# Optimization experiments

Hardware: AMD Instinct MI355X
Metric: run time of the kernel (lower is better)

Reference implementation:

```python
import jax, jax.numpy as jnp
import numpy as np


def _lstm(x_seq, Wih, Whh, bih, bhh, hidden):
    """Single-layer batch_first LSTM, PyTorch gate order (i,f,g,o).
    x_seq: [B, T, D_in]. Returns (outputs [B, T, H], h_T [B, H])."""
    B = x_seq.shape[0]
    h0 = jnp.zeros((B, hidden), x_seq.dtype)
    c0 = jnp.zeros((B, hidden), x_seq.dtype)

    def step(carry, x_t):
        h, c = carry
        gates = x_t @ Wih.T + bih + h @ Whh.T + bhh  # [B, 4H]
        i, f, g, o = jnp.split(gates, 4, axis=-1)
        i = jax.nn.sigmoid(i)
        f = jax.nn.sigmoid(f)
        g = jnp.tanh(g)
        o = jax.nn.sigmoid(o)
        c = f * c + i * g
        h = o * jnp.tanh(c)
        return (h, c), h

    (hT, _), hs = jax.lax.scan(step, (h0, c0), jnp.swapaxes(x_seq, 0, 1))
    return jnp.swapaxes(hs, 0, 1), hT


def setup_inputs() -> dict:
    key = jax.random.key(0)
    ks = jax.random.split(key, 20)
    B, T = 4096, 140
    W = 0.1  # weight scale to keep gates out of saturation
    inp = {"x": jax.random.normal(ks[0], (B, 1, T), jnp.float32)}
    shapes = {
        "Wih_e1": (512, 1), "Whh_e1": (512, 128), "bih_e1": (512,), "bhh_e1": (512,),
        "Wih_e2": (256, 128), "Whh_e2": (256, 64), "bih_e2": (256,), "bhh_e2": (256,),
        "Wih_d1": (512, 64), "Whh_d1": (512, 128), "bih_d1": (512,), "bhh_d1": (512,),
        "Wih_d2": (4, 128), "Whh_d2": (4, 1), "bih_d2": (4,), "bhh_d2": (4,),
    }
    for i, (name, shp) in enumerate(shapes.items()):
        inp[name] = jax.random.normal(ks[i + 1], shp, jnp.float32) * W
    return inp


def reference(x, Wih_e1, Whh_e1, bih_e1, bhh_e1,
              Wih_e2, Whh_e2, bih_e2, bhh_e2,
              Wih_d1, Whh_d1, bih_d1, bhh_d1,
              Wih_d2, Whh_d2, bih_d2, bhh_d2):
    T = 140
    # x: [B,1,140] -> [B,140,1]
    x_enc = x[:, 0, :, None]
    _, h1 = _lstm(x_enc, Wih_e1, Whh_e1, bih_e1, bhh_e1, 128)  # h1: [B,128]
    # faithful to original bug: hn1 [1,B,128] fed as batch_first input (batch=1, seq=B)
    hn1_seq = h1[None, :, :]
    _, z = _lstm(hn1_seq, Wih_e2, Whh_e2, bih_e2, bhh_e2, 64)  # z: [1,64]
    dec_in = jnp.broadcast_to(z[:, None, :], (1, T, 64))
    out1, _ = _lstm(dec_in, Wih_d1, Whh_d1, bih_d1, bhh_d1, 128)  # [1,140,128]
    out2, _ = _lstm(out1, Wih_d2, Whh_d2, bih_d2, bhh_d2, 1)      # [1,140,1]
    recon = out2[..., 0][:, None, :]  # [1,1,140]
    return recon
```

## Files before the change

kernel.cpp:

```cpp
#include <hip/hip_runtime.h>
#include <hip/hip_bf16.h>


typedef float v2f __attribute__((ext_vector_type(2)));

__device__ __forceinline__ v2f pk_fma(v2f a, v2f b, v2f c) {
  v2f d;
  asm("v_pk_fma_f32 %0, %1, %2, %3" : "=v"(d) : "v"(a), "v"(b), "v"(c));
  return d;
}

__device__ __forceinline__ float sigm(float x) {
  return 1.0f / (1.0f + __expf(-x));
}
__device__ __forceinline__ float tanh_fast(float x) {
  return 1.0f - 2.0f / (__expf(2.0f * x) + 1.0f);
}

__device__ __forceinline__ void wg_barrier() {
  asm volatile("s_waitcnt lgkmcnt(0)\n\ts_barrier" ::: "memory");
}

template <int CTRL>
__device__ __forceinline__ float dppmv(float v) {
  return __int_as_float(__builtin_amdgcn_update_dpp(
      0, __float_as_int(v), CTRL, 0xF, 0xF, true));
}
#define DPP_XOR1   0xB1
#define DPP_XOR2   0x4E
#define DPP_ROT1   0x93
#define DPP_HMIRR  0x141
#define DPP_MIRR   0x140

__device__ __forceinline__ int swzc(int k) { return k + ((k >> 5) << 2); }

#define A_BB 16

__global__ __launch_bounds__(512, 2) void lstm_e1_kernel(
    const float* __restrict__ x,
    const float* __restrict__ Wih,
    const float* __restrict__ Whh,
    const float* __restrict__ bih,
    const float* __restrict__ bhh,
    float* __restrict__ h1_out)
{
  const int j    = threadIdx.x;
  const int lane = j & 63;
  const int w    = j >> 6;
  const int u    = w * 16 + (lane >> 2);
  const int q    = lane & 3;
  const int b0   = blockIdx.x * A_BB;

  __shared__ float Hs[2][A_BB][144];
  __shared__ float xs[2][A_BB];

  for (int i = j; i < A_BB * 144; i += 512) ((float*)Hs[0])[i] = 0.0f;
  if (j < A_BB) xs[0][j] = x[(b0 + j) * 140];

  v2f wr2[4][16];
#pragma unroll
  for (int g = 0; g < 4; ++g)
#pragma unroll
    for (int k = 0; k < 32; k += 4) {
      const float4 t4 = *(const float4*)&Whh[(g * 128 + u) * 128 + q * 32 + k];
      wr2[g][k / 2 + 0].x = t4.x; wr2[g][k / 2 + 0].y = t4.y;
      wr2[g][k / 2 + 1].x = t4.z; wr2[g][k / 2 + 1].y = t4.w;
    }

  float wih[4], bs[4];
#pragma unroll
  for (int g = 0; g < 4; ++g) {
    wih[g] = Wih[g * 128 + u];
    bs[g]  = bih[g * 128 + u] + bhh[g * 128 + u];
  }

  float c[4]  = {0.f, 0.f, 0.f, 0.f};
  float hr[4] = {0.f, 0.f, 0.f, 0.f};
  __syncthreads();

  int cur = 0;
  for (int t = 0; t < 140; ++t) {
    const int nxt = cur ^ 1;

    v2f R2[4][4];
#pragma unroll
    for (int g = 0; g < 4; ++g)
#pragma unroll
      for (int i = 0; i < 4; ++i) { R2[g][i].x = 0.f; R2[g][i].y = 0.f; }

#pragma unroll
    for (int s = 0; s < 4; ++s) {
      if (s) {
#pragma unroll
        for (int g = 0; g < 4; ++g)
#pragma unroll
          for (int i = 0; i < 4; ++i) {
            R2[g][i].x = dppmv<DPP_ROT1>(R2[g][i].x);
            R2[g][i].y = dppmv<DPP_ROT1>(R2[g][i].y);
          }
      }
      const int cch = (q - 1 - s) & 3;
      const float* hbase = &Hs[cur][cch * 4][q * 36];
#pragma unroll
      for (int i = 0; i < 4; ++i) {
        const float* hrow = hbase + i * 144;
#pragma unroll
        for (int kk = 0; kk < 8; ++kk) {
          const float4 hv = *(const float4*)&hrow[kk * 4];
          v2f h01; h01.x = hv.x; h01.y = hv.y;
          v2f h23; h23.x = hv.z; h23.y = hv.w;
#pragma unroll
          for (int g = 0; g < 4; ++g) {
            R2[g][i] = pk_fma(wr2[g][2 * kk + 0], h01, R2[g][i]);
            R2[g][i] = pk_fma(wr2[g][2 * kk + 1], h23, R2[g][i]);
          }
        }
      }
    }

    if (j < A_BB && (t + 1) < 140) xs[nxt][j] = x[(b0 + j) * 140 + t + 1];

    const float4 xv = *(const float4*)&xs[cur][q * 4];
    const float xa[4] = {xv.x, xv.y, xv.z, xv.w};
#pragma unroll
    for (int i = 0; i < 4; ++i) {
      const float gi = sigm(R2[0][i].x + R2[0][i].y + __builtin_fmaf(wih[0], xa[i], bs[0]));
      const float gf = sigm(R2[1][i].x + R2[1][i].y + __builtin_fmaf(wih[1], xa[i], bs[1]));
      const float gg = tanh_fast(R2[2][i].x + R2[2][i].y + __builtin_fmaf(wih[2], xa[i], bs[2]));
      const float go = sigm(R2[3][i].x + R2[3][i].y + __builtin_fmaf(wih[3], xa[i], bs[3]));
      c[i]  = gf * c[i] + gi * gg;
      hr[i] = go * tanh_fast(c[i]);
      Hs[nxt][q * 4 + i][swzc(u)] = hr[i];
    }
    wg_barrier();
    cur = nxt;
  }

#pragma unroll
  for (int i = 0; i < 4; ++i)
    h1_out[(b0 + q * 4 + i) * 128 + u] = hr[i];
}

__global__ __launch_bounds__(256, 1) void u_pre_kernel(
    const float* __restrict__ h1,
    const float* __restrict__ Wih,
    const float* __restrict__ bih,
    const float* __restrict__ bhh,
    float* __restrict__ Up)
{
  const int t = blockIdx.x;
  const int j = threadIdx.x;
  __shared__ float hs[128];
  if (j < 128) hs[j] = h1[t * 128 + j];
  __syncthreads();
  float acc = bih[j] + bhh[j];
#pragma unroll
  for (int k = 0; k < 128; k += 4) {
    const float4 hv = *(const float4*)&hs[k];
    const float4 wv = *(const float4*)&Wih[j * 128 + k];
    acc += wv.x * hv.x + wv.y * hv.y + wv.z * hv.z + wv.w * hv.w;
  }
  Up[t * 256 + (j & 63) * 4 + (j >> 6)] = acc;
}

__global__ __launch_bounds__(128, 1) void lstm_e2_scan_kernel(
    const float4* __restrict__ Up,
    const float* __restrict__ Whh,
    float* __restrict__ z_out)
{
  const int j = threadIdx.x;
  const int u = j >> 1;
  const int p = j & 1;

  __shared__ float hb[2][64];

  v2f wr2[4][16];
#pragma unroll
  for (int g = 0; g < 4; ++g)
#pragma unroll
    for (int k = 0; k < 32; k += 4) {
      const float4 t4 = *(const float4*)&Whh[(g * 64 + u) * 64 + p * 32 + k];
      wr2[g][k / 2 + 0].x = t4.x; wr2[g][k / 2 + 0].y = t4.y;
      wr2[g][k / 2 + 1].x = t4.z; wr2[g][k / 2 + 1].y = t4.w;
    }

  if (j < 64) hb[0][j] = 0.0f;
  float c = 0.0f, h = 0.0f;

  float4 U0 = Up[0 * 64 + u];
  float4 U1 = Up[1 * 64 + u];
  __syncthreads();

  int cur = 0;
#pragma unroll 1
  for (int t = 0; t < 4096; t += 2) {
#pragma unroll
    for (int half = 0; half < 2; ++half) {
      const int tp = (t + 2 + half < 4096) ? (t + 2 + half) : 4095;
      const float4 Unew = Up[tp * 64 + u];
      const float4 Ucur = half ? U1 : U0;

      const float* hrow = &hb[cur][p * 32];
      v2f A0, A1, A2, A3;
      A0.x = 0.f; A0.y = 0.f; A1 = A0; A2 = A0; A3 = A0;
#pragma unroll
      for (int kk = 0; kk < 8; ++kk) {
        const float4 hv = *(const float4*)&hrow[kk * 4];
        v2f hx; hx.x = hv.x; hx.y = hv.y;
        v2f hy; hy.x = hv.z; hy.y = hv.w;
        A0 = pk_fma(wr2[0][2 * kk], hx, A0); A0 = pk_fma(wr2[0][2 * kk + 1], hy, A0);
        A1 = pk_fma(wr2[1][2 * kk], hx, A1); A1 = pk_fma(wr2[1][2 * kk + 1], hy, A1);
        A2 = pk_fma(wr2[2][2 * kk], hx, A2); A2 = pk_fma(wr2[2][2 * kk + 1], hy, A2);
        A3 = pk_fma(wr2[3][2 * kk], hx, A3); A3 = pk_fma(wr2[3][2 * kk + 1], hy, A3);
      }
      float a0 = A0.x + A0.y, a1 = A1.x + A1.y;
      float a2 = A2.x + A2.y, a3 = A3.x + A3.y;
      a0 += dppmv<DPP_XOR1>(a0);
      a1 += dppmv<DPP_XOR1>(a1);
      a2 += dppmv<DPP_XOR1>(a2);
      a3 += dppmv<DPP_XOR1>(a3);

      const float gi = sigm(a0 + Ucur.x);
      const float gf = sigm(a1 + Ucur.y);
      const float gg = tanh_fast(a2 + Ucur.z);
      const float go = sigm(a3 + Ucur.w);
      c = gf * c + gi * gg;
      h = go * tanh_fast(c);
      if (p == 0) hb[cur ^ 1][u] = h;
      if (half) U1 = Unew; else U0 = Unew;
      wg_barrier();
      cur ^= 1;
    }
  }
  if (p == 0) z_out[u] = h;
}

__global__ __launch_bounds__(512, 1) void lstm_dec_kernel(
    const float* __restrict__ z,
    const float* __restrict__ Wih1,
    const float* __restrict__ Whh1,
    const float* __restrict__ bih1,
    const float* __restrict__ bhh1,
    const float* __restrict__ Wih2,
    const float* __restrict__ Whh2,
    const float* __restrict__ bih2,
    const float* __restrict__ bhh2,
    float* __restrict__ out)
{
  const int j = threadIdx.x;
  const int u = j >> 2;
  const int q = j & 3;

  __shared__ float hd[2][144];
  __shared__ float zs[64];
  __shared__ float act4[4];

  if (j < 64) zs[j] = z[j];
  if (j < 144) hd[0][j] = 0.0f;
  __syncthreads();

  float wr[4][32];
#pragma unroll
  for (int g = 0; g < 4; ++g)
#pragma unroll
    for (int k = 0; k < 32; k += 4)
      *(float4*)&wr[g][k] = *(const float4*)&Whh1[(g * 128 + u) * 128 + q * 32 + k];

  float pre0[4];
#pragma unroll
  for (int g = 0; g < 4; ++g) {
    float acc = bih1[g * 128 + u] + bhh1[g * 128 + u];
#pragma unroll
    for (int k = 0; k < 64; k += 4) {
      const float4 zv = *(const float4*)&zs[k];
      const float4 wv = *(const float4*)&Wih1[(g * 128 + u) * 64 + k];
      acc += wv.x * zv.x + wv.y * zv.y + wv.z * zv.z + wv.w * zv.w;
    }
    pre0[g] = acc;
  }

  const int g2  = j >> 4;
  const int i16 = j & 15;
  float w2d[8] = {0,0,0,0,0,0,0,0};
  if (j < 64) {
#pragma unroll
    for (int e = 0; e < 8; ++e) w2d[e] = Wih2[g2 * 128 + i16 * 8 + e];
  }
  const float bb2_0 = bih2[0] + bhh2[0], wh2_0 = Whh2[0];
  const float bb2_1 = bih2[1] + bhh2[1], wh2_1 = Whh2[1];
  const float bb2_2 = bih2[2] + bhh2[2], wh2_2 = Whh2[2];
  const float bb2_3 = bih2[3] + bhh2[3], wh2_3 = Whh2[3];

  float c1 = 0.0f;
  float c2 = 0.0f, h2 = 0.0f;

  int cur = 0;
  for (int t = 0; t < 140; ++t) {
    float a0 = 0.f, a1 = 0.f, a2 = 0.f, a3 = 0.f;
#pragma unroll
    for (int kk = 0; kk < 8; ++kk) {
      const float4 hv = *(const float4*)&hd[cur][q * 36 + kk * 4];
      a0 = __builtin_fmaf(wr[0][kk*4+0], hv.x, a0); a0 = __builtin_fmaf(wr[0][kk*4+1], hv.y, a0);
      a0 = __builtin_fmaf(wr[0][kk*4+2], hv.z, a0); a0 = __builtin_fmaf(wr[0][kk*4+3], hv.w, a0);
      a1 = __builtin_fmaf(wr[1][kk*4+0], hv.x, a1); a1 = __builtin_fmaf(wr[1][kk*4+1], hv.y, a1);
      a1 = __builtin_fmaf(wr[1][kk*4+2], hv.z, a1); a1 = __builtin_fmaf(wr[1][kk*4+3], hv.w, a1);
      a2 = __builtin_fmaf(wr[2][kk*4+0], hv.x, a2); a2 = __builtin_fmaf(wr[2][kk*4+1], hv.y, a2);
      a2 = __builtin_fmaf(wr[2][kk*4+2], hv.z, a2); a2 = __builtin_fmaf(wr[2][kk*4+3], hv.w, a2);
      a3 = __builtin_fmaf(wr[3][kk*4+0], hv.x, a3); a3 = __builtin_fmaf(wr[3][kk*4+1], hv.y, a3);
      a3 = __builtin_fmaf(wr[3][kk*4+2], hv.z, a3); a3 = __builtin_fmaf(wr[3][kk*4+3], hv.w, a3);
    }
    a0 += dppmv<DPP_XOR1>(a0); a0 += dppmv<DPP_XOR2>(a0);
    a1 += dppmv<DPP_XOR1>(a1); a1 += dppmv<DPP_XOR2>(a1);
    a2 += dppmv<DPP_XOR1>(a2); a2 += dppmv<DPP_XOR2>(a2);
    a3 += dppmv<DPP_XOR1>(a3); a3 += dppmv<DPP_XOR2>(a3);

    const float gi = sigm(a0 + pre0[0]);
    const float gf = sigm(a1 + pre0[1]);
    const float gg = tanh_fast(a2 + pre0[2]);
    const float go = sigm(a3 + pre0[3]);
    c1 = gf * c1 + gi * gg;
    const float h1v = go * tanh_fast(c1);
    if (q == 0) hd[cur ^ 1][swzc(u)] = h1v;
    wg_barrier();
    cur ^= 1;

    if (j < 64) {
      const int kb = i16 * 8;
      const float4 hA = *(const float4*)&hd[cur][swzc(kb)];
      const float4 hB = *(const float4*)&hd[cur][swzc(kb) + 4];
      float p = hA.x * w2d[0];
      p = __builtin_fmaf(hA.y, w2d[1], p);
      p = __builtin_fmaf(hA.z, w2d[2], p);
      p = __builtin_fmaf(hA.w, w2d[3], p);
      p = __builtin_fmaf(hB.x, w2d[4], p);
      p = __builtin_fmaf(hB.y, w2d[5], p);
      p = __builtin_fmaf(hB.z, w2d[6], p);
      p = __builtin_fmaf(hB.w, w2d[7], p);
      p += dppmv<DPP_XOR1>(p);
      p += dppmv<DPP_XOR2>(p);
      p += dppmv<DPP_HMIRR>(p);
      p += dppmv<DPP_MIRR>(p);
      if (i16 == 0) act4[g2] = p;
      const float4 acts = *(const float4*)&act4[0];
      const float gi2 = sigm(acts.x + bb2_0 + wh2_0 * h2);
      const float gf2 = sigm(acts.y + bb2_1 + wh2_1 * h2);
      const float gg2 = tanh_fast(acts.z + bb2_2 + wh2_2 * h2);
      const float go2 = sigm(acts.w + bb2_3 + wh2_3 * h2);
      c2 = gf2 * c2 + gi2 * gg2;
      h2 = go2 * tanh_fast(c2);
      if (j == 0) out[t] = h2;
    }
  }
}

extern "C" void kernel_launch(void* const* d_in, const int* in_sizes, int n_in,
                              void* d_out, int out_size, void* d_ws, size_t ws_size,
                              hipStream_t stream) {
  const float* x      = (const float*)d_in[0];
  const float* Wih_e1 = (const float*)d_in[1];
  const float* Whh_e1 = (const float*)d_in[2];
  const float* bih_e1 = (const float*)d_in[3];
  const float* bhh_e1 = (const float*)d_in[4];
  const float* Wih_e2 = (const float*)d_in[5];
  const float* Whh_e2 = (const float*)d_in[6];
  const float* bih_e2 = (const float*)d_in[7];
  const float* bhh_e2 = (const float*)d_in[8];
  const float* Wih_d1 = (const float*)d_in[9];
  const float* Whh_d1 = (const float*)d_in[10];
  const float* bih_d1 = (const float*)d_in[11];
  const float* bhh_d1 = (const float*)d_in[12];
  const float* Wih_d2 = (const float*)d_in[13];
  const float* Whh_d2 = (const float*)d_in[14];
  const float* bih_d2 = (const float*)d_in[15];
  const float* bhh_d2 = (const float*)d_in[16];

  float* out = (float*)d_out;

  float* h1 = (float*)d_ws;
  float* Up = h1 + 4096 * 128;
  float* zb = Up + 4096 * 256;

  lstm_e1_kernel<<<4096 / A_BB, 512, 0, stream>>>(x, Wih_e1, Whh_e1, bih_e1, bhh_e1, h1);
  u_pre_kernel<<<4096, 256, 0, stream>>>(h1, Wih_e2, bih_e2, bhh_e2, Up);
  lstm_e2_scan_kernel<<<1, 128, 0, stream>>>((const float4*)Up, Whh_e2, zb);
  lstm_dec_kernel<<<1, 512, 0, stream>>>(zb, Wih_d1, Whh_d1, bih_d1, bhh_d1,
                                         Wih_d2, Whh_d2, bih_d2, bhh_d2, out);
}
```

Before: 3.424 ms.

## Stage e2 input projections into LDS via async double-buffered chunk loads

The e2 scan kernel no longer issues a per-step global load of the precomputed input projection into registers. It streams 32-step chunks of Up into a double-buffered LDS array with global_load_lds and waits on vmcnt before each chunk. Each chunk's steps are unrolled with constant LDS offsets, removing the per-step global latency and index arithmetic from the serial 4096-step critical path. This costs 64KB of LDS plus extra barriers at chunk boundaries. It relies on hand-written vmcnt counting being correct.

```diff
diff --git a/kernel.cpp b/kernel.cpp
--- a/kernel.cpp
+++ b/kernel.cpp
@@ -168,10 +168,13 @@
     const float* __restrict__ Whh,
     float* __restrict__ z_out)
 {
-  const int j = threadIdx.x;
-  const int u = j >> 1;
-  const int p = j & 1;
-
+  const int j    = threadIdx.x;
+  const int u    = j >> 1;
+  const int p    = j & 1;
+  const int w    = j >> 6;
+  const int lane = j & 63;
+
+  __shared__ float4 Uc[2][32][64];
   __shared__ float hb[2][64];
 
   v2f wr2[4][16];
@@ -184,54 +187,88 @@
       wr2[g][k / 2 + 1].x = t4.z; wr2[g][k / 2 + 1].y = t4.w;
     }
 
-  if (j < 64) hb[0][j] = 0.0f;
+  if (j < 64) { hb[0][j] = 0.0f; hb[1][j] = 0.0f; }
+
+#define STAGE(BUF, CK)                                                        \
+  {                                                                           \
+    const char* g_ = (const char*)Up + (CK) * 32768 + w * 1024 + lane * 16;   \
+    char* l_ = (char*)&Uc[0][0][0] + (BUF) * 32768 + w * 1024;                \
+    _Pragma("unroll")                                                         \
+    for (int i_ = 0; i_ < 16; ++i_)                                           \
+      __builtin_amdgcn_global_load_lds(                                       \
+          (const __attribute__((address_space(1))) unsigned int*)(g_ + i_ * 2048), \
+          (__attribute__((address_space(3))) unsigned int*)(l_ + i_ * 2048),  \
+          16, 0, 0);                                                          \
+  }
+
+  STAGE(0, 0)
+  __syncthreads();
+
   float c = 0.0f, h = 0.0f;
-
-  float4 U0 = Up[0 * 64 + u];
-  float4 U1 = Up[1 * 64 + u];
-  __syncthreads();
-
-  int cur = 0;
+  const char* ucol0 = (const char*)&Uc[0][0][u];
+  const char* hrd0  = (const char*)&hb[0][p * 32];
+  char*       hwr0  = (char*)&hb[0][u];
+
+#define SCAN_STEP(UB, S8)                                                     \
+  {                                                                           \
+    const float4 Ucur = *(const float4*)((UB) + (S8) * 1024);                 \
+    const float* hrow = (const float*)(hrd0 + ((S8) & 1) * 256);              \
+    v2f A0, A1, A2, A3;                                                       \
+    A0.x = 0.f; A0.y = 0.f; A1 = A0; A2 = A0; A3 = A0;                        \
+    _Pragma("unroll")                                                         \
+    for (int kk = 0; kk < 8; ++kk) {                                          \
+      const float4 hv = *(const float4*)&hrow[kk * 4];                        \
+      v2f hx; hx.x = hv.x; hx.y = hv.y;                                       \
+      v2f hy; hy.x = hv.z; hy.y = hv.w;                                       \
+      A0 = pk_fma(wr2[0][2 * kk], hx, A0); A0 = pk_fma(wr2[0][2 * kk + 1], hy, A0); \
+      A1 = pk_fma(wr2[1][2 * kk], hx, A1); A1 = pk_fma(wr2[1][2 * kk + 1], hy, A1); \
+      A2 = pk_fma(wr2[2][2 * kk], hx, A2); A2 = pk_fma(wr2[2][2 * kk + 1], hy, A2); \
+      A3 = pk_fma(wr2[3][2 * kk], hx, A3); A3 = pk_fma(wr2[3][2 * kk + 1], hy, A3); \
+    }                                                                         \
+    float a0 = A0.x + A0.y, a1 = A1.x + A1.y;                                 \
+    float a2 = A2.x + A2.y, a3 = A3.x + A3.y;                                 \
+    a0 += dppmv<DPP_XOR1>(a0); a1 += dppmv<DPP_XOR1>(a1);                     \
+    a2 += dppmv<DPP_XOR1>(a2); a3 += dppmv<DPP_XOR1>(a3);                     \
+    const float gi = sigm(a0 + Ucur.x);                                       \
+    const float gf = sigm(a1 + Ucur.y);                                       \
+    const float gg = tanh_fast(a2 + Ucur.z);                                  \
+    const float go = sigm(a3 + Ucur.w);                                       \
+    c = gf * c + gi * gg;                                                     \
+    h = go * tanh_fast(c);                                                    \
+    if (p == 0) *(float*)(hwr0 + (((S8) & 1) ^ 1) * 256) = h;                 \
+    wg_barrier();                                                             \
+  }
+
+#define CHUNK(BUF)                                                            \
+  {                                                                           \
+    const char* ub_ = ucol0 + (BUF) * 32768;                                  \
+    _Pragma("unroll 1")                                                       \
+    for (int s8o_ = 0; s8o_ < 4; ++s8o_) {                                    \
+      _Pragma("unroll")                                                       \
+      for (int s8i_ = 0; s8i_ < 8; ++s8i_) { SCAN_STEP(ub_, s8i_) }           \
+      ub_ += 8 * 1024;                                                        \
+    }                                                                         \
+  }
+
 #pragma unroll 1
-  for (int t = 0; t < 4096; t += 2) {
-#pragma unroll
-    for (int half = 0; half < 2; ++half) {
-      const int tp = (t + 2 + half < 4096) ? (t + 2 + half) : 4095;
-      const float4 Unew = Up[tp * 64 + u];
-      const float4 Ucur = half ? U1 : U0;
-
-      const float* hrow = &hb[cur][p * 32];
-      v2f A0, A1, A2, A3;
-      A0.x = 0.f; A0.y = 0.f; A1 = A0; A2 = A0; A3 = A0;
-#pragma unroll
-      for (int kk = 0; kk < 8; ++kk) {
-        const float4 hv = *(const float4*)&hrow[kk * 4];
-        v2f hx; hx.x = hv.x; hx.y = hv.y;
-        v2f hy; hy.x = hv.z; hy.y = hv.w;
-        A0 = pk_fma(wr2[0][2 * kk], hx, A0); A0 = pk_fma(wr2[0][2 * kk + 1], hy, A0);
-        A1 = pk_fma(wr2[1][2 * kk], hx, A1); A1 = pk_fma(wr2[1][2 * kk + 1], hy, A1);
-        A2 = pk_fma(wr2[2][2 * kk], hx, A2); A2 = pk_fma(wr2[2][2 * kk + 1], hy, A2);
-        A3 = pk_fma(wr2[3][2 * kk], hx, A3); A3 = pk_fma(wr2[3][2 * kk + 1], hy, A3);
-      }
-      float a0 = A0.x + A0.y, a1 = A1.x + A1.y;
-      float a2 = A2.x + A2.y, a3 = A3.x + A3.y;
-      a0 += dppmv<DPP_XOR1>(a0);
-      a1 += dppmv<DPP_XOR1>(a1);
-      a2 += dppmv<DPP_XOR1>(a2);
-      a3 += dppmv<DPP_XOR1>(a3);
-
-      const float gi = sigm(a0 + Ucur.x);
-      const float gf = sigm(a1 + Ucur.y);
-      const float gg = tanh_fast(a2 + Ucur.z);
-      const float go = sigm(a3 + Ucur.w);
-      c = gf * c + gi * gg;
-      h = go * tanh_fast(c);
-      if (p == 0) hb[cur ^ 1][u] = h;
-      if (half) U1 = Unew; else U0 = Unew;
-      wg_barrier();
-      cur ^= 1;
-    }
-  }
+  for (int ck2 = 0; ck2 < 64; ++ck2) {
+    STAGE(1, 2 * ck2 + 1)
+    asm volatile("s_waitcnt vmcnt(16)" ::: "memory");
+    __builtin_amdgcn_s_barrier();
+    CHUNK(0)
+    if (ck2 < 63) {
+      STAGE(0, 2 * ck2 + 2)
+      asm volatile("s_waitcnt vmcnt(16)" ::: "memory");
+    } else {
+      asm volatile("s_waitcnt vmcnt(0)" ::: "memory");
+    }
+    __builtin_amdgcn_s_barrier();
+    CHUNK(1)
+  }
+#undef CHUNK
+#undef SCAN_STEP
+#undef STAGE
+
   if (p == 0) z_out[u] = h;
 }
 
@@ -328,19 +365,19 @@
       const int kb = i16 * 8;
       const float4 hA = *(const float4*)&hd[cur][swzc(kb)];
       const float4 hB = *(const float4*)&hd[cur][swzc(kb) + 4];
-      float p = hA.x * w2d[0];
-      p = __builtin_fmaf(hA.y, w2d[1], p);
-      p = __builtin_fmaf(hA.z, w2d[2], p);
-      p = __builtin_fmaf(hA.w, w2d[3], p);
-      p = __builtin_fmaf(hB.x, w2d[4], p);
-      p = __builtin_fmaf(hB.y, w2d[5], p);
-      p = __builtin_fmaf(hB.z, w2d[6], p);
-      p = __builtin_fmaf(hB.w, w2d[7], p);
-      p += dppmv<DPP_XOR1>(p);
-      p += dppmv<DPP_XOR2>(p);
-      p += dppmv<DPP_HMIRR>(p);
-      p += dppmv<DPP_MIRR>(p);
-      if (i16 == 0) act4[g2] = p;
+      float pp = hA.x * w2d[0];
+      pp = __builtin_fmaf(hA.y, w2d[1], pp);
+      pp = __builtin_fmaf(hA.z, w2d[2], pp);
+      pp = __builtin_fmaf(hA.w, w2d[3], pp);
+      pp = __builtin_fmaf(hB.x, w2d[4], pp);
+      pp = __builtin_fmaf(hB.y, w2d[5], pp);
+      pp = __builtin_fmaf(hB.z, w2d[6], pp);
+      pp = __builtin_fmaf(hB.w, w2d[7], pp);
+      pp += dppmv<DPP_XOR1>(pp);
+      pp += dppmv<DPP_XOR2>(pp);
+      pp += dppmv<DPP_HMIRR>(pp);
+      pp += dppmv<DPP_MIRR>(pp);
+      if (i16 == 0) act4[g2] = pp;
       const float4 acts = *(const float4*)&act4[0];
       const float gi2 = sigm(acts.x + bb2_0 + wh2_0 * h2);
       const float gf2 = sigm(acts.y + bb2_1 + wh2_1 * h2);
```

After: 3.465 ms. Within noise of the previous version (+1.2%).
